# Kernel optimization log

Measured on AMD Instinct MI355X. Metric: run time of the kernel, lower is better.

The kernel has to match this reference:

```python
import jax, jax.numpy as jnp
import numpy as np

TAU = 1.0
EPS = 1e-5


def _gcn_sparse(x, src, dst, ew, W, b, n):
    # PyG GCNConv: add self-loops (weight 1), sym-normalize, aggregate src->dst
    deg = jax.ops.segment_sum(ew, dst, num_segments=n) + 1.0
    dinv = jnp.where(deg > 0, jax.lax.rsqrt(deg), 0.0)
    h = x @ W
    coef = dinv[src] * ew * dinv[dst]              # [E]
    out = jax.ops.segment_sum(h[src] * coef[:, None], dst, num_segments=n)
    out = out + h * (dinv * dinv)[:, None]         # self-loop term
    return out + b


def _gcn_dense(x, A, W, b):
    # x: [B,N,d], A: [B,N,N] with A[b,i,j] = weight of edge j->i
    n = A.shape[-1]
    Ah = A + jnp.eye(n, dtype=A.dtype)
    deg = Ah.sum(-1)
    dinv = jnp.where(deg > 0, jax.lax.rsqrt(deg), 0.0)
    An = dinv[:, :, None] * Ah * dinv[:, None, :]
    return jnp.einsum('bij,bjd->bid', An, x @ W) + b


def _bn_silu(x, g, be, axes):
    # BatchNorm over node axis (training-mode batch stats, biased var) + SiLU
    m = x.mean(axes, keepdims=True)
    v = x.var(axes, keepdims=True)
    return jax.nn.silu(g * (x - m) * jax.lax.rsqrt(v + EPS) + be)


def setup_inputs() -> dict:
    key = jax.random.key(0)
    ks = jax.random.split(key, 12)
    B, NPG, EPER = 32, 1024, 16384
    CIN, C, K1, K2, OUT = 64, 128, 128, 32, 10
    N, E = B * NPG, B * EPER
    ei = jax.random.randint(ks[0], (2, E), 0, NPG, dtype=jnp.int32)
    off = jnp.repeat(jnp.arange(B, dtype=jnp.int32) * NPG, EPER)
    edge_index = ei + off[None, :]
    x = jax.random.normal(ks[1], (N, CIN), jnp.float32)
    batch = jnp.repeat(jnp.arange(B, dtype=jnp.int32), NPG)
    batch_ptr = jnp.arange(B + 1, dtype=jnp.int32) * NPG
    p = lambda k, s: jax.random.normal(k, s, jnp.float32) * 0.05
    return dict(
        x=x, edge_index=edge_index, batch=batch, batch_ptr=batch_ptr,
        w1a=p(ks[2], (CIN, C)), b1a=jnp.zeros((C,)), g1a=jnp.ones((C,)), be1a=jnp.zeros((C,)),
        w1b=p(ks[3], (C, C)), b1b=jnp.zeros((C,)), g1b=jnp.ones((C,)), be1b=jnp.zeros((C,)),
        wp1=p(ks[4], (C, K1)), bp1=jnp.zeros((K1,)),
        w2a=p(ks[5], (C, C)), b2a=jnp.zeros((C,)), g2a=jnp.ones((C,)), be2a=jnp.zeros((C,)),
        w2b=p(ks[6], (C, C)), b2b=jnp.zeros((C,)), g2b=jnp.ones((C,)), be2b=jnp.zeros((C,)),
        wp2=p(ks[7], (C, K2)), bp2=jnp.zeros((K2,)),
        wl=p(ks[8], (C, OUT)), bl=jnp.zeros((OUT,)))


def reference(x, edge_index, batch, batch_ptr,
              w1a, b1a, g1a, be1a, w1b, b1b, g1b, be1b, wp1, bp1,
              w2a, b2a, g2a, be2a, w2b, b2b, g2b, be2b, wp2, bp2,
              wl, bl):
    n = x.shape[0]
    B = batch_ptr.shape[0] - 1
    npg = n // B                                    # uniform nodes per graph
    src, dst = edge_index[0], edge_index[1]
    ew = jnp.ones((edge_index.shape[1],), x.dtype)  # edge_weight=None -> ones

    # ---- stack 1: sparse GCN residual blocks + stochastic pool ----
    h = _bn_silu(_gcn_sparse(x, src, dst, ew, w1a, b1a, n), g1a, be1a, 0)
    h = h + _bn_silu(_gcn_sparse(h, src, dst, ew, w1b, b1b, n), g1b, be1b, 0)
    s = jax.nn.softmax(_gcn_sparse(h, src, dst, ew, wp1, bp1, n) / TAU, -1)  # [n,K1]
    s3 = s.reshape(B, npg, -1)
    x2 = jnp.einsum('bnc,bnd->bcd', s3, h.reshape(B, npg, -1))   # s^T x  [B,K1,C]
    t = jax.ops.segment_sum(s[src] * ew[:, None], dst, num_segments=n)  # A s
    A2 = jnp.einsum('bnc,bnk->bck', s3, t.reshape(B, npg, -1))   # s^T A s [B,K1,K1]

    # ---- stack 2: dense GCN on pooled graph + stochastic pool ----
    h2 = _bn_silu(_gcn_dense(x2, A2, w2a, b2a), g2a, be2a, (0, 1))
    h2 = h2 + _bn_silu(_gcn_dense(h2, A2, w2b, b2b), g2b, be2b, (0, 1))
    s2 = jax.nn.softmax(_gcn_dense(h2, A2, wp2, bp2) / TAU, -1)  # [B,K1,K2]
    x3 = jnp.einsum('bnc,bnd->bcd', s2, h2)                      # [B,K2,C]

    # global mean pool over nodes per graph, linear, log_softmax
    g = x3.mean(axis=1)
    out = jax.nn.log_softmax(g @ wl + bl, axis=1)
    # aux losses are multiplied by 0 in the original forward -> exact zero
    return (out, jnp.zeros((), x.dtype))
```

## Files before the change

### kernel.cpp

```cpp
#include <hip/hip_runtime.h>
#include <cmath>

#define KSPLIT 16
#define ELL_ST 80

typedef __attribute__((ext_vector_type(8))) short short8;
typedef __attribute__((ext_vector_type(4))) float float4v;

static __device__ __forceinline__ unsigned short f2bf(float f){
  union { float f; unsigned u; } c; c.f = f;
  unsigned r = c.u + 0x7fff + ((c.u >> 16) & 1);
  return (unsigned short)(r >> 16);
}
static __device__ __forceinline__ float u2f(unsigned u){
  union { unsigned u; float f; } c; c.u = u; return c.f;
}
static __device__ __forceinline__ float silu(float y){ return y/(1.f+__expf(-y)); }

static __device__ __forceinline__ void coef_prologue(const float* __restrict__ stats,
                                                     const float* __restrict__ gamma,
                                                     const float* __restrict__ beta,
                                                     float invM, float* lds, int tbase){
  int t = threadIdx.x - tbase;
  if(t >= 0 && t < 128){
    float s = 0.f, q = 0.f;
    #pragma unroll
    for(int k=0;k<8;k++){ s += stats[k*128+t]; q += stats[1024 + k*128+t]; }
    float m = s*invM;
    float v = q*invM - m*m;
    float sc = gamma[t]*rsqrtf(v + 1e-5f);
    lds[t] = sc;
    lds[128+t] = beta[t] - m*sc;
  }
}

__global__ void k_fill_ell(const int* __restrict__ src, const int* __restrict__ dst,
                           int* __restrict__ cursor, int* __restrict__ esrc, int E){
  int e = blockIdx.x*256 + threadIdx.x;
  if(e<E){
    int d = dst[e];
    int p = atomicAdd(&cursor[d], 1);
    if(p < ELL_ST) esrc[(size_t)d*ELL_ST + p] = src[e];
  }
}

__global__ void k_dinv_wt(const int* __restrict__ deg, float* __restrict__ dinv, int n,
                          const float* __restrict__ w1a, const float* __restrict__ w1b,
                          const float* __restrict__ wp1, unsigned short* __restrict__ t1a,
                          unsigned short* __restrict__ t1b, unsigned short* __restrict__ tp1,
                          int CIN){
  int i = blockIdx.x*256 + threadIdx.x;
  if(i < n){ dinv[i] = rsqrtf((float)deg[i] + 1.0f); }
  int j = i - n;
  int n1 = CIN*128, n2 = 128*128;
  if(j >= 0 && j < n1){
    int k = j >> 7, c = j & 127;
    t1a[(size_t)c*CIN + k] = f2bf(w1a[j]);
  } else if(j >= n1 && j < n1+n2){
    int jj = j - n1; int k = jj >> 7, c = jj & 127;
    t1b[(size_t)c*128 + k] = f2bf(w1b[jj]);
  } else if(j >= n1+n2 && j < n1+2*n2){
    int jj = j - n1 - n2; int k = jj >> 7, c = jj & 127;
    tp1[(size_t)c*128 + k] = f2bf(wp1[jj]);
  }
}

__global__ void k_gemm_mfma(const float* __restrict__ A, const float* __restrict__ A2,
                            const unsigned short* __restrict__ Bt,
                            unsigned short* __restrict__ Cb, int M, int K, int Nc,
                            const float* __restrict__ rowscale,
                            const float* __restrict__ stA, const float* __restrict__ gA,
                            const float* __restrict__ beA,
                            const float* __restrict__ stB, const float* __restrict__ gB,
                            const float* __restrict__ beB, float invM){
  __shared__ unsigned short Abf[64][40];
  __shared__ unsigned short Bbf[64][40];
  __shared__ float lcA[256], lcB[256];
  int tid = threadIdx.x;
  if(stA) coef_prologue(stA, gA, beA, invM, lcA, 0);
  if(stB) coef_prologue(stB, gB, beB, invM, lcB, 128);
  if(stA || stB) __syncthreads();
  int wv = tid >> 6, lane = tid & 63;
  int quad = lane >> 4, l16 = lane & 15;
  int row0 = blockIdx.y*64, col0 = blockIdx.x*64;
  int sr = tid >> 2, sk = (tid & 3)*8;
  float4v acc[4] = {};
  for(int kt=0; kt<K; kt+=32){
    const float* ap = &A[(size_t)(row0+sr)*K + kt + sk];
    float va[8];
    *(float4*)&va[0] = *(const float4*)ap;
    *(float4*)&va[4] = *(const float4*)(ap+4);
    if(stB){
      const float* bp = &A2[(size_t)(row0+sr)*K + kt + sk];
      float vb[8];
      *(float4*)&vb[0] = *(const float4*)bp;
      *(float4*)&vb[4] = *(const float4*)(bp+4);
      #pragma unroll
      for(int i=0;i<8;i++){
        int c = kt+sk+i;
        va[i] = silu(lcA[c]*va[i] + lcA[128+c]) + silu(lcB[c]*vb[i] + lcB[128+c]);
      }
    } else if(stA){
      #pragma unroll
      for(int i=0;i<8;i++){
        int c = kt+sk+i;
        va[i] = silu(lcA[c]*va[i] + lcA[128+c]);
      }
    }
    uint4 pk;
    pk.x = (unsigned)f2bf(va[0]) | ((unsigned)f2bf(va[1])<<16);
    pk.y = (unsigned)f2bf(va[2]) | ((unsigned)f2bf(va[3])<<16);
    pk.z = (unsigned)f2bf(va[4]) | ((unsigned)f2bf(va[5])<<16);
    pk.w = (unsigned)f2bf(va[6]) | ((unsigned)f2bf(va[7])<<16);
    *(uint4*)&Abf[sr][sk] = pk;
    *(uint4*)&Bbf[sr][sk] = *(const uint4*)&Bt[(size_t)(col0+sr)*K + kt + sk];
    __syncthreads();
    short8 af = *(const short8*)&Abf[wv*16 + l16][quad*8];
    #pragma unroll
    for(int t=0;t<4;t++){
      short8 bf = *(const short8*)&Bbf[t*16 + l16][quad*8];
      acc[t] = __builtin_amdgcn_mfma_f32_16x16x32_bf16(af, bf, acc[t], 0, 0, 0);
    }
    __syncthreads();
  }
  float scr[4];
  #pragma unroll
  for(int r=0;r<4;r++){
    int grow = row0 + wv*16 + quad*4 + r;
    scr[r] = rowscale ? rowscale[grow] : 1.f;
  }
  #pragma unroll
  for(int t=0;t<4;t++){
    #pragma unroll
    for(int r=0;r<4;r++){
      int grow = row0 + wv*16 + quad*4 + r;
      int gcol = col0 + t*16 + l16;
      Cb[(size_t)grow*Nc + gcol] = f2bf(acc[t][r]*scr[r]);
    }
  }
}

__global__ void k_gemm64(const float* __restrict__ A, const float* __restrict__ B,
                         float* __restrict__ C, int M, int K, int Nc,
                         const float* __restrict__ rowscale,
                         const float* __restrict__ stA, const float* __restrict__ gA,
                         const float* __restrict__ beA, float invM){
  __shared__ float As[16][68];
  __shared__ float Bs[16][68];
  __shared__ float lc[256];
  int tid = threadIdx.x;
  if(stA){ coef_prologue(stA, gA, beA, invM, lc, 0); __syncthreads(); }
  int tx = tid & 15, ty = tid >> 4;
  int row0 = blockIdx.y*64, col0 = blockIdx.x*64;
  float acc[4][4] = {};
  for(int kt=0; kt<K; kt+=16){
    int ra = tid >> 2, ka = (tid & 3)*4;
    float4 va = *(const float4*)&A[(size_t)(row0+ra)*K + kt + ka];
    if(stA){
      float vv[4] = {va.x, va.y, va.z, va.w};
      #pragma unroll
      for(int i=0;i<4;i++){
        int c = kt+ka+i;
        vv[i] = silu(lc[c]*vv[i] + lc[128+c]);
      }
      va.x=vv[0]; va.y=vv[1]; va.z=vv[2]; va.w=vv[3];
    }
    As[ka+0][ra]=va.x; As[ka+1][ra]=va.y; As[ka+2][ra]=va.z; As[ka+3][ra]=va.w;
    int rb = tid >> 4, cb = (tid & 15)*4;
    *(float4*)&Bs[rb][cb] = *(const float4*)&B[(size_t)(kt+rb)*Nc + col0 + cb];
    __syncthreads();
    #pragma unroll
    for(int k=0;k<16;k++){
      float4 a = *(const float4*)&As[k][ty*4];
      float4 b = *(const float4*)&Bs[k][tx*4];
      float av[4]={a.x,a.y,a.z,a.w}, bv[4]={b.x,b.y,b.z,b.w};
      #pragma unroll
      for(int i=0;i<4;i++)
        #pragma unroll
        for(int j=0;j<4;j++) acc[i][j] += av[i]*bv[j];
    }
    __syncthreads();
  }
  #pragma unroll
  for(int i=0;i<4;i++){
    int r = row0 + ty*4 + i;
    float sc = rowscale ? rowscale[r] : 1.0f;
    float4 v; v.x=acc[i][0]*sc; v.y=acc[i][1]*sc; v.z=acc[i][2]*sc; v.w=acc[i][3]*sc;
    *(float4*)&C[(size_t)r*Nc + col0 + tx*4] = v;
  }
}

template<bool DO_SOFTMAX, bool GCN, bool STATS, bool BF16IN>
__global__ void k_gather(const int* __restrict__ degc, const int* __restrict__ esrc,
                         const float* __restrict__ dinv, const void* __restrict__ hWs,
                         const float* __restrict__ bias, float* __restrict__ out,
                         float* __restrict__ stats){
  __shared__ float lsum[4][128];
  __shared__ float lsq[4][128];
  const unsigned short* h16 = (const unsigned short*)hWs;
  const float* h32 = (const float*)hWs;
  int wave = threadIdx.x >> 6;
  int lane = threadIdx.x & 63;
  int bid = blockIdx.x;
  int d = ((bid & 7) << 12) | ((bid >> 3) << 2) | wave;
  int grp = lane >> 5;
  int c4 = (lane & 31)*4;
  int cnt = degc[d]; if(cnt > ELL_ST) cnt = ELL_ST;
  const int* row = esrc + (size_t)d*ELL_ST;

  auto loadrow = [&](int s)->float4{
    if(BF16IN){
      uint2 u = *(const uint2*)&h16[(size_t)s*128 + c4];
      float4 v;
      v.x = u2f(u.x << 16); v.y = u2f(u.x & 0xffff0000u);
      v.z = u2f(u.y << 16); v.w = u2f(u.y & 0xffff0000u);
      return v;
    } else {
      return *(const float4*)&h32[(size_t)s*128 + c4];
    }
  };

  float4 a0 = {0.f,0.f,0.f,0.f}, a1 = {0.f,0.f,0.f,0.f};
  float4 a2 = {0.f,0.f,0.f,0.f}, a3 = {0.f,0.f,0.f,0.f};
  if(GCN && grp == 0)
    a0 = loadrow(d);
  for(int base=0; base<cnt; base+=32){
    int m = cnt - base; if(m > 32) m = 32;
    int idx = (lane < m) ? row[base + lane] : 0;
    for(int j0 = 0; j0 < m; j0 += 8){
      int jj0 = j0+grp, jj1 = j0+grp+2, jj2 = j0+grp+4, jj3 = j0+grp+6;
      int s0 = __shfl(idx, jj0 < m ? jj0 : 0);
      int s1 = __shfl(idx, jj1 < m ? jj1 : 0);
      int s2 = __shfl(idx, jj2 < m ? jj2 : 0);
      int s3 = __shfl(idx, jj3 < m ? jj3 : 0);
      if(jj0 < m){ float4 v = loadrow(s0);
        a0.x+=v.x; a0.y+=v.y; a0.z+=v.z; a0.w+=v.w; }
      if(jj1 < m){ float4 v = loadrow(s1);
        a1.x+=v.x; a1.y+=v.y; a1.z+=v.z; a1.w+=v.w; }
      if(jj2 < m){ float4 v = loadrow(s2);
        a2.x+=v.x; a2.y+=v.y; a2.z+=v.z; a2.w+=v.w; }
      if(jj3 < m){ float4 v = loadrow(s3);
        a3.x+=v.x; a3.y+=v.y; a3.z+=v.z; a3.w+=v.w; }
    }
  }
  float4 acc;
  acc.x = (a0.x+a1.x)+(a2.x+a3.x);
  acc.y = (a0.y+a1.y)+(a2.y+a3.y);
  acc.z = (a0.z+a1.z)+(a2.z+a3.z);
  acc.w = (a0.w+a1.w)+(a2.w+a3.w);
  acc.x += __shfl_xor(acc.x, 32);
  acc.y += __shfl_xor(acc.y, 32);
  acc.z += __shfl_xor(acc.z, 32);
  acc.w += __shfl_xor(acc.w, 32);
  float4 val = acc;
  if(GCN){
    float dv = dinv[d];
    float4 bi = *(const float4*)&bias[c4];
    val.x = dv*acc.x + bi.x; val.y = dv*acc.y + bi.y;
    val.z = dv*acc.z + bi.z; val.w = dv*acc.w + bi.w;
  }
  if(DO_SOFTMAX){
    float mx = fmaxf(fmaxf(val.x,val.y), fmaxf(val.z,val.w));
    #pragma unroll
    for(int o=1;o<32;o<<=1) mx = fmaxf(mx, __shfl_xor(mx,o));
    float4 e; e.x=__expf(val.x-mx); e.y=__expf(val.y-mx);
    e.z=__expf(val.z-mx); e.w=__expf(val.w-mx);
    float s = e.x+e.y+e.z+e.w;
    #pragma unroll
    for(int o=1;o<32;o<<=1) s += __shfl_xor(s,o);
    float inv = 1.f/s;
    val.x=e.x*inv; val.y=e.y*inv; val.z=e.z*inv; val.w=e.w*inv;
  }
  if(grp == 0)
    *(float4*)&out[(size_t)d*128 + c4] = val;
  if(STATS){
    if(grp == 0){
      *(float4*)&lsum[wave][c4] = val;
      float4 q; q.x=val.x*val.x; q.y=val.y*val.y; q.z=val.z*val.z; q.w=val.w*val.w;
      *(float4*)&lsq[wave][c4] = q;
    }
    __syncthreads();
    int t = threadIdx.x;
    if(t < 128){
      float s = (lsum[0][t]+lsum[1][t]) + (lsum[2][t]+lsum[3][t]);
      atomicAdd(&stats[(bid & 7)*128 + t], s);
    } else {
      int c = t - 128;
      float q = (lsq[0][c]+lsq[1][c]) + (lsq[2][c]+lsq[3][c]);
      atomicAdd(&stats[1024 + (bid & 7)*128 + c], q);
    }
  }
}

template<bool FUSED>
__global__ __launch_bounds__(256, 2)
void k_pool_split(const float* __restrict__ P, const float* __restrict__ Qa,
                  const float* __restrict__ Qb,
                  const float* __restrict__ stA, const float* __restrict__ gA,
                  const float* __restrict__ beA,
                  const float* __restrict__ stB, const float* __restrict__ gB,
                  const float* __restrict__ beB, float invM,
                  float* __restrict__ part, int npg, int nb){
  __shared__ float Ps[2][8][132], Qs[2][8][132];
  __shared__ float lcA[256], lcB[256];
  int tid = threadIdx.x;
  if(FUSED){
    coef_prologue(stA, gA, beA, invM, lcA, 0);
    coef_prologue(stB, gB, beB, invM, lcB, 128);
    __syncthreads();
  }
  int ks = blockIdx.x, b = blockIdx.y;
  int klen = npg / KSPLIT;
  size_t base = ((size_t)b*npg + (size_t)ks*klen)*128;
  int tx = tid & 15, ty = tid >> 4;
  int r = tid >> 5, c4s = (tid & 31)*4;
  size_t off = (size_t)r*128 + c4s;

  auto stage_q = [&](float4 qa, float4 qb)->float4{
    float4 q;
    if(FUSED){
      q.x = silu(lcA[c4s+0]*qa.x+lcA[128+c4s+0]) + silu(lcB[c4s+0]*qb.x+lcB[128+c4s+0]);
      q.y = silu(lcA[c4s+1]*qa.y+lcA[128+c4s+1]) + silu(lcB[c4s+1]*qb.y+lcB[128+c4s+1]);
      q.z = silu(lcA[c4s+2]*qa.z+lcA[128+c4s+2]) + silu(lcB[c4s+2]*qb.z+lcB[128+c4s+2]);
      q.w = silu(lcA[c4s+3]*qa.w+lcA[128+c4s+3]) + silu(lcB[c4s+3]*qb.w+lcB[128+c4s+3]);
    } else q = qa;
    return q;
  };

  {
    float4 p0 = *(const float4*)&P[base + off];
    float4 qa0 = *(const float4*)&Qa[base + off];
    float4 qb0 = FUSED ? *(const float4*)&Qb[base + off] : qa0;
    *(float4*)&Ps[0][r][c4s] = p0;
    *(float4*)&Qs[0][r][c4s] = stage_q(qa0, qb0);
  }
  __syncthreads();

  float acc[8][8] = {};
  int chunks = klen >> 3;
  for(int c=0; c<chunks; c++){
    float4 pn, qan, qbn;
    if(c+1 < chunks){
      size_t nb2 = base + (size_t)((c+1)*8)*128 + off;
      pn  = *(const float4*)&P[nb2];
      qan = *(const float4*)&Qa[nb2];
      if(FUSED) qbn = *(const float4*)&Qb[nb2];
    }
    int cb = c & 1;
    #pragma unroll
    for(int k=0;k<8;k++){
      float4 a0 = *(const float4*)&Ps[cb][k][ty*4];
      float4 a1 = *(const float4*)&Ps[cb][k][64+ty*4];
      float4 b0 = *(const float4*)&Qs[cb][k][tx*4];
      float4 b1 = *(const float4*)&Qs[cb][k][64+tx*4];
      float av[8]={a0.x,a0.y,a0.z,a0.w,a1.x,a1.y,a1.z,a1.w};
      float bv[8]={b0.x,b0.y,b0.z,b0.w,b1.x,b1.y,b1.z,b1.w};
      #pragma unroll
      for(int i=0;i<8;i++)
        #pragma unroll
        for(int j=0;j<8;j++) acc[i][j] += av[i]*bv[j];
    }
    if(c+1 < chunks){
      int nbuf = (c+1) & 1;
      *(float4*)&Ps[nbuf][r][c4s] = pn;
      *(float4*)&Qs[nbuf][r][c4s] = stage_q(qan, FUSED ? qbn : qan);
    }
    __syncthreads();
  }

  float* outp = part + ((size_t)(ks*nb + b)*128)*128;
  #pragma unroll
  for(int ih=0; ih<2; ih++)
    #pragma unroll
    for(int ii=0; ii<4; ii++){
      int i = ih*64 + ty*4 + ii;
      #pragma unroll
      for(int jh=0; jh<2; jh++){
        float4 v;
        v.x = acc[ih*4+ii][jh*4+0];
        v.y = acc[ih*4+ii][jh*4+1];
        v.z = acc[ih*4+ii][jh*4+2];
        v.w = acc[ih*4+ii][jh*4+3];
        *(float4*)&outp[(size_t)i*128 + jh*64 + tx*4] = v;
      }
    }
}

__global__ void k_pool_reduce2(const float* __restrict__ p1, const float* __restrict__ p2,
                               float* __restrict__ x2, float* __restrict__ A2,
                               float* __restrict__ dinv2, int total){
  int i = blockIdx.x*256 + threadIdx.x;
  int half = total >> 2;
  if(i < half){
    float4 s = *(const float4*)&p1[(size_t)i*4];
    #pragma unroll
    for(int ks=1; ks<KSPLIT; ks++){
      float4 v = *(const float4*)&p1[(size_t)ks*total + (size_t)i*4];
      s.x+=v.x; s.y+=v.y; s.z+=v.z; s.w+=v.w;
    }
    *(float4*)&x2[(size_t)i*4] = s;
  } else {
    int ia = i - half;
    float4 s = *(const float4*)&p2[(size_t)ia*4];
    #pragma unroll
    for(int ks=1; ks<KSPLIT; ks++){
      float4 v = *(const float4*)&p2[(size_t)ks*total + (size_t)ia*4];
      s.x+=v.x; s.y+=v.y; s.z+=v.z; s.w+=v.w;
    }
    *(float4*)&A2[(size_t)ia*4] = s;
    float rs = s.x+s.y+s.z+s.w;
    #pragma unroll
    for(int o=16;o>0;o>>=1) rs += __shfl_xor(rs, o);
    if((threadIdx.x & 31) == 0) dinv2[ia>>5] = rsqrtf(rs + 1.0f);
  }
}

__global__ void k_bgemm_post_stats(const float* __restrict__ A, const float* __restrict__ X,
                                   const float* __restrict__ dinv2, const float* __restrict__ bias,
                                   float* __restrict__ outp, float* __restrict__ stats){
  __shared__ float As[16][17], Xs[16][17];
  __shared__ float rs[16][17], rq[16][17];
  int b = blockIdx.z;
  int i0 = blockIdx.y*16, j0 = blockIdx.x*16;
  int tx = threadIdx.x, ty = threadIdx.y;
  const float* Ab = A + (size_t)b*16384;
  const float* Xb = X + (size_t)b*16384;
  float acc = 0.f;
  for(int k0=0;k0<128;k0+=16){
    As[ty][tx] = Ab[(i0+ty)*128 + k0+tx];
    Xs[ty][tx] = Xb[(k0+ty)*128 + j0+tx];
    __syncthreads();
    #pragma unroll
    for(int k=0;k<16;k++) acc += As[ty][k]*Xs[k][tx];
    __syncthreads();
  }
  int gr = b*128 + i0 + ty;
  float v = dinv2[gr]*(acc + Xb[(i0+ty)*128 + j0+tx]) + bias[j0+tx];
  outp[(size_t)gr*128 + j0+tx] = v;
  rs[ty][tx] = v; rq[ty][tx] = v*v;
  __syncthreads();
  if(ty == 0){
    float s = 0.f, q = 0.f;
    #pragma unroll
    for(int k=0;k<16;k++){ s += rs[k][tx]; q += rq[k][tx]; }
    int slot = b & 7;
    atomicAdd(&stats[slot*128 + j0+tx], s);
    atomicAdd(&stats[1024 + slot*128 + j0+tx], q);
  }
}

__global__ void k_final_reduce(const float* __restrict__ dTa, const float* __restrict__ dTb,
                               const float* __restrict__ stA, const float* __restrict__ gA,
                               const float* __restrict__ beA,
                               const float* __restrict__ stB, const float* __restrict__ gB,
                               const float* __restrict__ beB, float invMc,
                               float* __restrict__ g, int K1n, int Cc, float inv_k2){
  __shared__ float red[256];
  __shared__ float lcA[256], lcB[256];
  coef_prologue(stA, gA, beA, invMc, lcA, 0);
  coef_prologue(stB, gB, beB, invMc, lcB, 128);
  __syncthreads();
  int b = blockIdx.y;
  int n0 = blockIdx.x*16;
  int tid = threadIdx.x;
  int c = tid & 127, rh = tid >> 7;
  const float* pa = dTa + ((size_t)b*K1n + n0)*Cc;
  const float* pb = dTb + ((size_t)b*K1n + n0)*Cc;
  float sa = lcA[c], ha = lcA[128+c], sb = lcB[c], hb = lcB[128+c];
  float acc = 0.f;
  for(int r = rh; r < 16; r += 2){
    float ya = sa*pa[(size_t)r*Cc + c] + ha;
    float yb = sb*pb[(size_t)r*Cc + c] + hb;
    acc += silu(ya) + silu(yb);
  }
  red[tid] = acc;
  __syncthreads();
  if(tid < 128)
    atomicAdd(&g[b*128 + c], (red[tid] + red[tid+128]) * inv_k2);
}

__global__ void k_final3(const float* __restrict__ g, const float* __restrict__ wl,
                         const float* __restrict__ bl, float* __restrict__ out,
                         int Cc, int OUTc, int zero_idx){
  int b = blockIdx.x;
  int t = threadIdx.x;
  __shared__ float logits[32];
  __shared__ float mred, lred;
  const float* gb = g + b*Cc;
  if(t < OUTc){
    float l = bl[t];
    for(int d=0; d<Cc; d++) l += gb[d]*wl[d*OUTc + t];
    logits[t] = l;
  }
  __syncthreads();
  if(t==0){
    float m = -1e30f;
    for(int o=0;o<OUTc;o++) m = fmaxf(m, logits[o]);
    float s = 0.f;
    for(int o=0;o<OUTc;o++) s += __expf(logits[o]-m);
    mred = m; lred = logf(s);
  }
  __syncthreads();
  if(t < OUTc) out[b*OUTc + t] = logits[t] - mred - lred;
  if(b==0 && t==0 && zero_idx >= 0) out[zero_idx] = 0.f;
}

extern "C" void kernel_launch(void* const* d_in, const int* in_sizes, int n_in,
                              void* d_out, int out_size, void* d_ws, size_t ws_size,
                              hipStream_t stream){
  const float* x    = (const float*)d_in[0];
  const int*   ei   = (const int*)d_in[1];
  const float* w1a  = (const float*)d_in[4];
  const float* b1a  = (const float*)d_in[5];
  const float* g1a  = (const float*)d_in[6];
  const float* be1a = (const float*)d_in[7];
  const float* w1b  = (const float*)d_in[8];
  const float* b1b  = (const float*)d_in[9];
  const float* g1b  = (const float*)d_in[10];
  const float* be1b = (const float*)d_in[11];
  const float* wp1  = (const float*)d_in[12];
  const float* bp1  = (const float*)d_in[13];
  const float* w2a  = (const float*)d_in[14];
  const float* b2a  = (const float*)d_in[15];
  const float* g2a  = (const float*)d_in[16];
  const float* be2a = (const float*)d_in[17];
  const float* w2b  = (const float*)d_in[18];
  const float* b2b  = (const float*)d_in[19];
  const float* g2b  = (const float*)d_in[20];
  const float* be2b = (const float*)d_in[21];
  const float* wl   = (const float*)d_in[24];
  const float* bl   = (const float*)d_in[25];
  float* out = (float*)d_out;

  const int C_   = in_sizes[5];
  const int CIN_ = in_sizes[4]/C_;
  const int N    = in_sizes[0]/CIN_;
  const int E    = in_sizes[1]/2;
  const int B_   = in_sizes[3]-1;
  const int NPG_ = N/B_;
  const int K1_  = in_sizes[13];
  const int K2_  = in_sizes[23];
  const int OUTc = in_sizes[25];
  const int M2   = B_*K1_;
  const int total = M2*C_;

  const int* srcI = ei;
  const int* dstI = ei + E;

  float* ws = (float*)d_ws;
  size_t o = 0;
  float* dinv  = ws + o; o += (size_t)N;
  unsigned short* bufW = (unsigned short*)(ws + o); o += (size_t)N*C_/2;
  float* bufA  = ws + o; o += (size_t)N*C_;
  float* bufB  = ws + o; o += (size_t)N*C_;
  float* bufS  = ws + o; o += (size_t)N*C_;
  float* bufT  = ws + o; o += (size_t)N*C_;
  float* x2    = ws + o; o += (size_t)total;
  float* A2    = ws + o; o += (size_t)total;
  float* dinv2 = ws + o; o += (size_t)M2;
  float* st1a  = ws + o; o += 2048;
  float* st1b  = ws + o; o += 2048;
  float* stDa  = ws + o; o += 2048;
  float* stDb  = ws + o; o += 2048;
  float* gbuf  = ws + o; o += (size_t)B_*C_;
  int* cursor  = (int*)(ws + o); o += (size_t)N;
  float* part  = ws + o; o += (size_t)KSPLIT*total;
  float* part2 = ws + o; o += (size_t)KSPLIT*total;
  float* dW  = part;
  float* dTa = part + (size_t)total;
  float* dTb = part + 2*(size_t)total;
  unsigned short* wt1a = (unsigned short*)(ws + o); o += (size_t)CIN_*C_/2 + 64;
  unsigned short* wt1b = (unsigned short*)(ws + o); o += (size_t)C_*C_/2 + 64;
  unsigned short* wtp1 = (unsigned short*)(ws + o); o += (size_t)C_*C_/2 + 64;
  int* esrc    = (int*)(ws + o); o += (size_t)N*ELL_ST;
  (void)ws_size; (void)n_in;

  dim3 blk256(256);
  dim3 gblk(16,16);
  auto g1 = [](int n){ return dim3((unsigned)((n+255)/256)); };
  const float invN = 1.0f/N, invM2 = 1.0f/M2;

  hipMemsetAsync(st1a, 0, (4*2048 + (size_t)B_*C_)*sizeof(float) + (size_t)N*sizeof(int), stream);
  k_fill_ell<<<g1(E), blk256, 0, stream>>>(srcI, dstI, cursor, esrc, E);
  k_dinv_wt<<<g1(N + CIN_*C_ + 2*C_*C_), blk256, 0, stream>>>(cursor, dinv, N,
      w1a, w1b, wp1, wt1a, wt1b, wtp1, CIN_);

  dim3 gath((unsigned)(N/4));

  k_gemm_mfma<<<dim3(C_/64, N/64), blk256, 0, stream>>>(x, nullptr, wt1a, bufW, N, CIN_, C_, dinv,
      nullptr, nullptr, nullptr, nullptr, nullptr, nullptr, 0.f);
  k_gather<false,true,true,true><<<gath, blk256, 0, stream>>>(cursor, esrc, dinv, bufW, b1a, bufA, st1a);

  k_gemm_mfma<<<dim3(C_/64, N/64), blk256, 0, stream>>>(bufA, nullptr, wt1b, bufW, N, C_, C_, dinv,
      st1a, g1a, be1a, nullptr, nullptr, nullptr, invN);
  k_gather<false,true,true,true><<<gath, blk256, 0, stream>>>(cursor, esrc, dinv, bufW, b1b, bufB, st1b);

  k_gemm_mfma<<<dim3(K1_/64, N/64), blk256, 0, stream>>>(bufA, bufB, wtp1, bufW, N, C_, K1_, dinv,
      st1a, g1a, be1a, st1b, g1b, be1b, invN);
  k_gather<true,true,false,true><<<gath, blk256, 0, stream>>>(cursor, esrc, dinv, bufW, bp1, bufS, nullptr);
  k_gather<false,false,false,false><<<gath, blk256, 0, stream>>>(cursor, esrc, nullptr, bufS, nullptr, bufT, nullptr);

  k_pool_split<true><<<dim3(KSPLIT, B_), blk256, 0, stream>>>(bufS, bufA, bufB,
      st1a, g1a, be1a, st1b, g1b, be1b, invN, part, NPG_, B_);
  k_pool_split<false><<<dim3(KSPLIT, B_), blk256, 0, stream>>>(bufS, bufT, nullptr,
      nullptr, nullptr, nullptr, nullptr, nullptr, nullptr, 0.f, part2, NPG_, B_);
  k_pool_reduce2<<<g1(total/2), blk256, 0, stream>>>(part, part2, x2, A2, dinv2, total);

  k_gemm64<<<dim3(C_/64, M2/64), blk256, 0, stream>>>(x2, w2a, dW, M2, C_, C_, dinv2,
      nullptr, nullptr, nullptr, 0.f);
  k_bgemm_post_stats<<<dim3(C_/16, K1_/16, B_), gblk, 0, stream>>>(A2, dW, dinv2, b2a, dTa, stDa);

  k_gemm64<<<dim3(C_/64, M2/64), blk256, 0, stream>>>(dTa, w2b, dW, M2, C_, C_, dinv2,
      stDa, g2a, be2a, invM2);
  k_bgemm_post_stats<<<dim3(C_/16, K1_/16, B_), gblk, 0, stream>>>(A2, dW, dinv2, b2b, dTb, stDb);

  int zero_idx = (out_size > B_*OUTc) ? B_*OUTc : -1;
  k_final_reduce<<<dim3(K1_/16, B_), blk256, 0, stream>>>(dTa, dTb,
      stDa, g2a, be2a, stDb, g2b, be2b, invM2, gbuf, K1_, C_, 1.0f/K2_);
  k_final3<<<dim3((unsigned)B_), dim3(128), 0, stream>>>(gbuf, wl, bl, out, C_, OUTc, zero_idx);
}
```

Measured before the change: 393.1 us.

## Merge pool-split kernels into one launch, halve K-split, unroll gather fast path

The two pooling split kernels (S^T h and S^T A S) become a single launch, with blockIdx.z choosing the fused-BN path or the plain path. KSPLIT drops from 16 to 8, so there are fewer partial products to write and reduce, but each block does more work. The gather kernel gains an unguarded inner loop over full groups of 8 edges and makes the edge count wave-uniform via readfirstlane. The fused pool kernel now branches on a runtime flag instead of a template parameter, which may raise register pressure.

Result: faster. 375.5 us (-4.5%).

```diff
diff --git a/kernel.cpp b/kernel.cpp
--- a/kernel.cpp
+++ b/kernel.cpp
@@ -1,7 +1,7 @@
 #include <hip/hip_runtime.h>
 #include <cmath>
 
-#define KSPLIT 16
+#define KSPLIT 8
 #define ELL_ST 80
 
 typedef __attribute__((ext_vector_type(8))) short short8;
@@ -206,6 +206,7 @@
   int grp = lane >> 5;
   int c4 = (lane & 31)*4;
   int cnt = degc[d]; if(cnt > ELL_ST) cnt = ELL_ST;
+  cnt = __builtin_amdgcn_readfirstlane(cnt);
   const int* row = esrc + (size_t)d*ELL_ST;
 
   auto loadrow = [&](int s)->float4{
@@ -227,7 +228,23 @@
   for(int base=0; base<cnt; base+=32){
     int m = cnt - base; if(m > 32) m = 32;
     int idx = (lane < m) ? row[base + lane] : 0;
-    for(int j0 = 0; j0 < m; j0 += 8){
+    int full = m & ~7;
+    int j0 = 0;
+    for(; j0 < full; j0 += 8){
+      int s0 = __shfl(idx, j0+grp);
+      int s1 = __shfl(idx, j0+grp+2);
+      int s2 = __shfl(idx, j0+grp+4);
+      int s3 = __shfl(idx, j0+grp+6);
+      float4 v0 = loadrow(s0);
+      float4 v1 = loadrow(s1);
+      float4 v2 = loadrow(s2);
+      float4 v3 = loadrow(s3);
+      a0.x+=v0.x; a0.y+=v0.y; a0.z+=v0.z; a0.w+=v0.w;
+      a1.x+=v1.x; a1.y+=v1.y; a1.z+=v1.z; a1.w+=v1.w;
+      a2.x+=v2.x; a2.y+=v2.y; a2.z+=v2.z; a2.w+=v2.w;
+      a3.x+=v3.x; a3.y+=v3.y; a3.z+=v3.z; a3.w+=v3.w;
+    }
+    if(j0 < m){
       int jj0 = j0+grp, jj1 = j0+grp+2, jj2 = j0+grp+4, jj3 = j0+grp+6;
       int s0 = __shfl(idx, jj0 < m ? jj0 : 0);
       int s1 = __shfl(idx, jj1 < m ? jj1 : 0);
@@ -292,19 +309,19 @@
   }
 }
 
-template<bool FUSED>
 __global__ __launch_bounds__(256, 2)
-void k_pool_split(const float* __restrict__ P, const float* __restrict__ Qa,
-                  const float* __restrict__ Qb,
-                  const float* __restrict__ stA, const float* __restrict__ gA,
-                  const float* __restrict__ beA,
-                  const float* __restrict__ stB, const float* __restrict__ gB,
-                  const float* __restrict__ beB, float invM,
-                  float* __restrict__ part, int npg, int nb){
+void k_pool2(const float* __restrict__ P, const float* __restrict__ Qa,
+             const float* __restrict__ Qb, const float* __restrict__ Qc,
+             const float* __restrict__ stA, const float* __restrict__ gA,
+             const float* __restrict__ beA,
+             const float* __restrict__ stB, const float* __restrict__ gB,
+             const float* __restrict__ beB, float invM,
+             float* __restrict__ part1, float* __restrict__ part2, int npg, int nb){
   __shared__ float Ps[2][8][132], Qs[2][8][132];
   __shared__ float lcA[256], lcB[256];
   int tid = threadIdx.x;
-  if(FUSED){
+  bool fused = (blockIdx.z == 0);
+  if(fused){
     coef_prologue(stA, gA, beA, invM, lcA, 0);
     coef_prologue(stB, gB, beB, invM, lcB, 128);
     __syncthreads();
@@ -315,10 +332,11 @@
   int tx = tid & 15, ty = tid >> 4;
   int r = tid >> 5, c4s = (tid & 31)*4;
   size_t off = (size_t)r*128 + c4s;
+  const float* Q1 = fused ? Qa : Qc;
 
   auto stage_q = [&](float4 qa, float4 qb)->float4{
     float4 q;
-    if(FUSED){
+    if(fused){
       q.x = silu(lcA[c4s+0]*qa.x+lcA[128+c4s+0]) + silu(lcB[c4s+0]*qb.x+lcB[128+c4s+0]);
       q.y = silu(lcA[c4s+1]*qa.y+lcA[128+c4s+1]) + silu(lcB[c4s+1]*qb.y+lcB[128+c4s+1]);
       q.z = silu(lcA[c4s+2]*qa.z+lcA[128+c4s+2]) + silu(lcB[c4s+2]*qb.z+lcB[128+c4s+2]);
@@ -329,8 +347,8 @@
 
   {
     float4 p0 = *(const float4*)&P[base + off];
-    float4 qa0 = *(const float4*)&Qa[base + off];
-    float4 qb0 = FUSED ? *(const float4*)&Qb[base + off] : qa0;
+    float4 qa0 = *(const float4*)&Q1[base + off];
+    float4 qb0 = fused ? *(const float4*)&Qb[base + off] : qa0;
     *(float4*)&Ps[0][r][c4s] = p0;
     *(float4*)&Qs[0][r][c4s] = stage_q(qa0, qb0);
   }
@@ -343,8 +361,8 @@
     if(c+1 < chunks){
       size_t nb2 = base + (size_t)((c+1)*8)*128 + off;
       pn  = *(const float4*)&P[nb2];
-      qan = *(const float4*)&Qa[nb2];
-      if(FUSED) qbn = *(const float4*)&Qb[nb2];
+      qan = *(const float4*)&Q1[nb2];
+      if(fused) qbn = *(const float4*)&Qb[nb2];
     }
     int cb = c & 1;
     #pragma unroll
@@ -363,12 +381,12 @@
     if(c+1 < chunks){
       int nbuf = (c+1) & 1;
       *(float4*)&Ps[nbuf][r][c4s] = pn;
-      *(float4*)&Qs[nbuf][r][c4s] = stage_q(qan, FUSED ? qbn : qan);
-    }
-    __syncthreads();
-  }
-
-  float* outp = part + ((size_t)(ks*nb + b)*128)*128;
+      *(float4*)&Qs[nbuf][r][c4s] = stage_q(qan, fused ? qbn : qan);
+    }
+    __syncthreads();
+  }
+
+  float* outp = (fused ? part1 : part2) + ((size_t)(ks*nb + b)*128)*128;
   #pragma unroll
   for(int ih=0; ih<2; ih++)
     #pragma unroll
@@ -600,10 +618,8 @@
   k_gather<true,true,false,true><<<gath, blk256, 0, stream>>>(cursor, esrc, dinv, bufW, bp1, bufS, nullptr);
   k_gather<false,false,false,false><<<gath, blk256, 0, stream>>>(cursor, esrc, nullptr, bufS, nullptr, bufT, nullptr);
 
-  k_pool_split<true><<<dim3(KSPLIT, B_), blk256, 0, stream>>>(bufS, bufA, bufB,
-      st1a, g1a, be1a, st1b, g1b, be1b, invN, part, NPG_, B_);
-  k_pool_split<false><<<dim3(KSPLIT, B_), blk256, 0, stream>>>(bufS, bufT, nullptr,
-      nullptr, nullptr, nullptr, nullptr, nullptr, nullptr, 0.f, part2, NPG_, B_);
+  k_pool2<<<dim3(KSPLIT, B_, 2), blk256, 0, stream>>>(bufS, bufA, bufB, bufT,
+      st1a, g1a, be1a, st1b, g1b, be1b, invN, part, part2, NPG_, B_);
   k_pool_reduce2<<<g1(total/2), blk256, 0, stream>>>(part, part2, x2, A2, dinv2, total);
 
   k_gemm64<<<dim3(C_/64, M2/64), blk256, 0, stream>>>(x2, w2a, dW, M2, C_, C_, dinv2,
```
